# Kernel tuning notes

Hardware: AMD Instinct MI355X
Metric: run time of the kernel (lower is better)

The kernel has to match this reference:

```python
import jax, jax.numpy as jnp
import numpy as np

H = 16
LN_EPS = 1e-5


def setup_inputs() -> dict:
    key = jax.random.key(0)
    ks = jax.random.split(key, 8)
    B, N, D = 2, 2048, 1024
    s = D ** -0.5
    return {
        "q_s": jax.random.normal(ks[0], (B, N, D), jnp.float32),
        "pos_emb": jax.random.normal(ks[1], (B, N, D), jnp.float32),
        "Wq": jax.random.normal(ks[2], (D, D), jnp.float32) * s,
        "Wk": jax.random.normal(ks[3], (D, D), jnp.float32) * s,
        "Wv": jax.random.normal(ks[4], (D, D), jnp.float32) * s,
        "Wo": jax.random.normal(ks[5], (D, D), jnp.float32) * s,
        "bo": jnp.zeros((D,), jnp.float32),
        "ln_g": jnp.ones((D,), jnp.float32),
        "ln_b": jnp.zeros((D,), jnp.float32),
    }


def _split_heads(t):
    b, n, d = t.shape
    return t.reshape(b, n, H, d // H).transpose(0, 2, 1, 3)  # b h n d


def reference(q_s, pos_emb, Wq, Wk, Wv, Wo, bo, ln_g, ln_b):
    # self-attention: k_s = v_s = q_s
    q = _split_heads(q_s @ Wq)
    k = _split_heads(q_s @ Wk)
    v = _split_heads(q_s @ Wv)
    p = _split_heads(pos_emb)
    scale = q.shape[-1] ** -0.5
    # content-content + content-position attention logits: [b,h,i,j]
    att = (jnp.einsum('bhid,bhjd->bhij', q, k) + jnp.einsum('bhid,bhjd->bhij', q, p)) * scale
    att = jax.nn.softmax(att, axis=-1)
    o = jnp.einsum('bhij,bhjd->bhid', att, v)
    b, h, n, d = o.shape
    o = o.transpose(0, 2, 1, 3).reshape(b, n, h * d)
    o = o @ Wo + bo  # out_layer (dropout rate 0 -> identity)
    x = o + q_s  # residual
    mu = jnp.mean(x, axis=-1, keepdims=True)
    var = jnp.var(x, axis=-1, keepdims=True)
    return (x - mu) * jax.lax.rsqrt(var + LN_EPS) * ln_g + ln_b
```

## Files before the change

kernel.cpp:

```cpp
#include <hip/hip_runtime.h>
#include <hip/hip_bf16.h>
#include <stdint.h>

typedef unsigned short u16;
typedef unsigned int u32;
typedef short s16x8 __attribute__((ext_vector_type(8)));
typedef short s16x4 __attribute__((ext_vector_type(4)));
typedef float f32x4 __attribute__((ext_vector_type(4)));

#define MFMA(a, b, c) __builtin_amdgcn_mfma_f32_16x16x32_bf16((a), (b), (c), 0, 0, 0)

__device__ __forceinline__ float bf2f(u16 h) {
  u32 u = ((u32)h) << 16;
  float f;
  __builtin_memcpy(&f, &u, 4);
  return f;
}

__device__ __forceinline__ u16 f2bf_rte(float f) {
  __hip_bfloat16 h = __float2bfloat16(f);
  u16 u;
  __builtin_memcpy(&u, &h, 2);
  return u;
}

__device__ __forceinline__ void gload16(const u16* g, u16* l) {
  __builtin_amdgcn_global_load_lds((const __attribute__((address_space(1))) u32*)g,
                                   (__attribute__((address_space(3))) u32*)l, 16, 0, 0);
}

__global__ __launch_bounds__(256) void k_cvt(const float* __restrict__ in,
                                             u16* __restrict__ out, int n8) {
  int i = blockIdx.x * 256 + threadIdx.x;
  if (i >= n8) return;
  const f32x4* p = (const f32x4*)(in + (size_t)i * 8);
  f32x4 a = p[0], b = p[1];
  s16x8 o;
  for (int k = 0; k < 4; ++k) o[k] = (short)f2bf_rte(a[k]);
  for (int k = 0; k < 4; ++k) o[4 + k] = (short)f2bf_rte(b[k]);
  *(s16x8*)(out + (size_t)i * 8) = o;
}

__global__ __launch_bounds__(256) void k_prep_pos(const float* __restrict__ pos,
                                                  u16* __restrict__ Pp) {
  const int t = threadIdx.x;
  const int bh = blockIdx.y, b = bh >> 4, h = bh & 15;
  const int n = blockIdx.x * 64 + (t >> 2);
  const int d0 = (t & 3) * 16;
  const float* src = &pos[((size_t)(b * 2048 + n)) * 1024 + h * 64 + d0];
  u16* dst = &Pp[((size_t)bh * 2048 + n) * 64 + d0];
  f32x4 a = *(const f32x4*)src;
  f32x4 bq = *(const f32x4*)(src + 4);
  f32x4 c = *(const f32x4*)(src + 8);
  f32x4 dq = *(const f32x4*)(src + 12);
  s16x8 o0, o1;
  for (int i = 0; i < 4; ++i) {
    o0[i] = (short)f2bf_rte(a[i]);
    o0[4 + i] = (short)f2bf_rte(bq[i]);
    o1[i] = (short)f2bf_rte(c[i]);
    o1[4 + i] = (short)f2bf_rte(dq[i]);
  }
  *(s16x8*)dst = o0;
  *(s16x8*)(dst + 8) = o1;
}

__global__ __launch_bounds__(256) void k_transpose_w(const float* __restrict__ W0,
                                                     const float* __restrict__ W1,
                                                     const float* __restrict__ W2,
                                                     const float* __restrict__ W3,
                                                     u16* __restrict__ out) {
  const int z = blockIdx.z;
  const float* in = (z == 0) ? W0 : (z == 1) ? W1 : (z == 2) ? W2 : W3;
  u16* o = out + (size_t)z * 1024 * 1024;
  __shared__ u16 tile[64][65];
  const int t = threadIdx.x, tx = t & 63, ty = t >> 6;
  const int r0 = blockIdx.y * 64, c0 = blockIdx.x * 64;
  for (int rr = 0; rr < 16; ++rr) {
    int row = rr * 4 + ty;
    tile[row][tx] = f2bf_rte(in[(size_t)(r0 + row) * 1024 + c0 + tx]);
  }
  __syncthreads();
  for (int rr = 0; rr < 16; ++rr) {
    int row = rr * 4 + ty;
    o[(size_t)(c0 + row) * 1024 + r0 + tx] = tile[tx][row];
  }
}

__global__ __launch_bounds__(256) void k_transpose_v(const u16* __restrict__ V,
                                                     u16* __restrict__ Vt) {
  __shared__ u16 tile[64][65];
  const int t = threadIdx.x, tx = t & 63, ty = t >> 6;
  const int j0 = blockIdx.x * 64;
  const int bh = blockIdx.y;
  const u16* src = V + (size_t)bh * 2048 * 64;
  u16* dst = Vt + (size_t)bh * 64 * 2048;
  for (int rr = 0; rr < 16; ++rr) {
    int row = rr * 4 + ty;
    tile[row][tx] = src[(size_t)(j0 + row) * 64 + tx];
  }
  __syncthreads();
  for (int rr = 0; rr < 16; ++rr) {
    int d = rr * 4 + ty;
    dst[(size_t)d * 2048 + j0 + tx] = tile[tx][d];
  }
}

__global__ __launch_bounds__(256) void k_qkv_gemm(const u16* __restrict__ X,
                                                  const u16* __restrict__ WT,
                                                  const u16* __restrict__ Pp,
                                                  u16* __restrict__ Qh,
                                                  u16* __restrict__ Kh,
                                                  u16* __restrict__ Vh) {
  __shared__ u16 As[3][4096];
  __shared__ u16 Bs[3][4096];
  const int t = threadIdx.x;
  const int lane = t & 63, wid = t >> 6;
  const int wr = wid >> 1, wc = wid & 1;
  const int g = lane >> 4, lr = lane & 15;
  const int lin = blockIdx.y * 24 + blockIdx.x;
  const int swz = (lin & 7) * 96 + (lin >> 3);
  const int m0 = (swz / 24) * 128, n0 = (swz % 24) * 128;

  const int srcRow = t >> 2;
  const int srcKsw = ((t & 3) * 8) ^ (((t >> 3) & 3) << 3);
  const u16* aSrc = &X[(size_t)(m0 + srcRow) * 1024 + srcKsw];
  const u16* bSrc = &WT[(size_t)(n0 + srcRow) * 1024 + srcKsw];

  const int csw = (g * 8) ^ (((lr >> 1) & 3) << 3);

  f32x4 acc[4][4] = {};

#define QKV_STAGE(buf, k0)                                   \
  {                                                          \
    gload16(aSrc + (k0), &As[buf][wid * 512]);               \
    gload16(aSrc + 65536 + (k0), &As[buf][wid * 512 + 2048]);\
    gload16(bSrc + (k0), &Bs[buf][wid * 512]);               \
    gload16(bSrc + 65536 + (k0), &Bs[buf][wid * 512 + 2048]);\
  }

  QKV_STAGE(0, 0);
  QKV_STAGE(1, 32);
  QKV_STAGE(2, 64);
  for (int k = 0; k < 32; ++k) {
    if (k < 30) {
      asm volatile("s_waitcnt vmcnt(8)" ::: "memory");
    } else if (k == 30) {
      asm volatile("s_waitcnt vmcnt(4)" ::: "memory");
    } else {
      asm volatile("s_waitcnt vmcnt(0)" ::: "memory");
    }
    __builtin_amdgcn_sched_barrier(0);
    __builtin_amdgcn_s_barrier();
    const int cur = k % 3;
    s16x8 a[4], b[4];
#pragma unroll
    for (int mi = 0; mi < 4; ++mi)
      a[mi] = *(const s16x8*)&As[cur][(wr * 64 + mi * 16 + lr) * 32 + csw];
#pragma unroll
    for (int nj = 0; nj < 4; ++nj)
      b[nj] = *(const s16x8*)&Bs[cur][(wc * 64 + nj * 16 + lr) * 32 + csw];
#pragma unroll
    for (int mi = 0; mi < 4; ++mi)
#pragma unroll
      for (int nj = 0; nj < 4; ++nj)
        acc[mi][nj] = MFMA(a[mi], b[nj], acc[mi][nj]);
    __builtin_amdgcn_s_barrier();
    if (k < 29) QKV_STAGE(cur, (k + 3) * 32);
  }
#undef QKV_STAGE

  const float QSCALE = 0.125f * 1.44269504f;
  for (int mi = 0; mi < 4; ++mi) {
    for (int nj = 0; nj < 4; ++nj) {
      const int n_g = n0 + wc * 64 + nj * 16 + lr;
      const int buf = n_g >> 10;
      const int col = n_g & 1023;
      const int h = col >> 6, d = col & 63;
      u16* dst = (buf == 0) ? Qh : ((buf == 1) ? Kh : Vh);
      for (int r = 0; r < 4; ++r) {
        const int row = m0 + wr * 64 + mi * 16 + g * 4 + r;
        const int b = row >> 11, n = row & 2047;
        const size_t off = (size_t)((b * 16 + h) * 2048 + n) * 64 + d;
        float v = acc[mi][nj][r];
        if (buf == 1) v += bf2f(Pp[off]);
        if (buf == 0) v *= QSCALE;
        dst[off] = f2bf_rte(v);
      }
    }
  }
}

__global__ __launch_bounds__(512, 4) void k_attn(const u16* __restrict__ Qh,
                                                 const u16* __restrict__ Kh,
                                                 const u16* __restrict__ Vt,
                                                 u16* __restrict__ Oh) {
  const int t = threadIdx.x, lane = t & 63, wid = t >> 6;
  const int g = lane >> 4, lr = lane & 15;
  const int hid = blockIdx.x;
  const int lid = (hid & 7) * 64 + (hid >> 3);
  const int bh = lid >> 4, itile = lid & 15;
  const int i0 = itile * 128 + wid * 16;

  __shared__ char Ks[4][8192];
  __shared__ char Vs[4][8192];

  const u16* Qp = Qh + (size_t)bh * 2048 * 64;
  const u16* Kp = Kh + (size_t)bh * 2048 * 64;
  const u16* Vp = Vt + (size_t)bh * 64 * 2048;

  s16x8 aq[2];
  aq[0] = *(const s16x8*)&Qp[(size_t)(i0 + lr) * 64 + g * 8];
  aq[1] = *(const s16x8*)&Qp[(size_t)(i0 + lr) * 64 + 32 + g * 8];

  f32x4 oa[4] = {};
  float ms = -1e30f, ls = 0.f;

  const int srow = t >> 3;
  const int sch = (t & 7) * 16;
  const int schS = sch ^ ((srow & 7) << 4);
  const u16* kB = &Kp[(size_t)srow * 64 + (schS >> 1)];
  const u16* vB = &Vp[(size_t)srow * 2048 + (schS >> 1)];

#define ATTN_STAGE(p)                                          \
  {                                                            \
    gload16(kB + (size_t)(p) * 4096, (u16*)Ks[(p) & 3] + wid * 512); \
    gload16(vB + (size_t)(p) * 64, (u16*)Vs[(p) & 3] + wid * 512);   \
  }

  ATTN_STAGE(0);
  ATTN_STAGE(1);
  ATTN_STAGE(2);

  for (int tt = 0; tt < 32; ++tt) {
    if (tt < 30) {
      asm volatile("s_waitcnt vmcnt(4)" ::: "memory");
    } else if (tt == 30) {
      asm volatile("s_waitcnt vmcnt(2)" ::: "memory");
    } else {
      asm volatile("s_waitcnt vmcnt(0)" ::: "memory");
    }
    __builtin_amdgcn_sched_barrier(0);
    __builtin_amdgcn_s_barrier();
    if (tt < 29) ATTN_STAGE(tt + 3);

    const char* Kc = Ks[tt & 3];
    const char* Vc = Vs[tt & 3];

    f32x4 s[4] = {};
    __builtin_amdgcn_s_setprio(1);
#pragma unroll
    for (int jf = 0; jf < 4; ++jf) {
      const int row = jf * 16 + lr;
      const int bw = (row & 7) << 4;
      s16x8 bk0 = *(const s16x8*)(Kc + ((row * 128 + g * 16) ^ bw));
      s16x8 bk1 = *(const s16x8*)(Kc + ((row * 128 + 64 + g * 16) ^ bw));
      s[jf] = MFMA(bk0, aq[0], s[jf]);
      s[jf] = MFMA(bk1, aq[1], s[jf]);
    }
    __builtin_amdgcn_s_setprio(0);

    float tl = s[0][0];
#pragma unroll
    for (int jf = 0; jf < 4; ++jf)
#pragma unroll
      for (int r = 0; r < 4; ++r)
        if (jf | r) tl = fmaxf(tl, s[jf][r]);
    if (!__all(tl <= ms + 8.f)) {
      float tm = fmaxf(tl, __shfl_xor(tl, 16, 64));
      tm = fmaxf(tm, __shfl_xor(tm, 32, 64));
      float mn = fmaxf(ms, tm);
      float al = __builtin_amdgcn_exp2f(ms - mn);
      ls *= al;
      ms = mn;
#pragma unroll
      for (int r = 0; r < 4; ++r) {
        float ab = __shfl(al, g * 4 + r, 64);
#pragma unroll
        for (int df = 0; df < 4; ++df) oa[df][r] *= ab;
      }
    }

#pragma unroll
    for (int jf = 0; jf < 4; ++jf)
#pragma unroll
      for (int r = 0; r < 4; ++r) {
        float p = __builtin_amdgcn_exp2f(s[jf][r] - ms);
        s[jf][r] = p;
        ls += p;
      }

    u32 pk[4][2];
#pragma unroll
    for (int jf = 0; jf < 4; ++jf) {
      asm("v_cvt_pk_bf16_f32 %0, %1, %2" : "=v"(pk[jf][0]) : "v"(s[jf][0]), "v"(s[jf][1]));
      asm("v_cvt_pk_bf16_f32 %0, %1, %2" : "=v"(pk[jf][1]) : "v"(s[jf][2]), "v"(s[jf][3]));
    }

    s16x8 pa[2];
#pragma unroll
    for (int c = 0; c < 2; ++c) {
      u32 w_[4];
#pragma unroll
      for (int wl = 0; wl < 2; ++wl) {
        u32 A = pk[2 * c][wl], B = pk[2 * c + 1][wl];
        asm("v_permlane32_swap_b32 %0, %1" : "+v"(A), "+v"(B));
        asm("v_permlane16_swap_b32 %0, %1" : "+v"(A), "+v"(B));
        w_[wl] = A;
        w_[2 + wl] = B;
      }
      __builtin_memcpy(&pa[c], w_, 16);
    }

    __builtin_amdgcn_s_setprio(1);
#pragma unroll
    for (int df = 0; df < 4; ++df) {
      const int row = df * 16 + lr;
      const int bw = (row & 7) << 4;
      s16x8 bv0 = *(const s16x8*)(Vc + ((row * 128 + g * 16) ^ bw));
      s16x8 bv1 = *(const s16x8*)(Vc + ((row * 128 + 64 + g * 16) ^ bw));
      oa[df] = MFMA(pa[0], bv0, oa[df]);
      oa[df] = MFMA(pa[1], bv1, oa[df]);
    }
    __builtin_amdgcn_s_setprio(0);
  }
#undef ATTN_STAGE

  ls += __shfl_xor(ls, 16, 64);
  ls += __shfl_xor(ls, 32, 64);
  float lb[4];
#pragma unroll
  for (int r = 0; r < 4; ++r) lb[r] = __shfl(ls, g * 4 + r, 64);

  u16* Op = Oh + (size_t)bh * 2048 * 64;
#pragma unroll
  for (int df = 0; df < 4; ++df)
#pragma unroll
    for (int r = 0; r < 4; ++r) {
      const int row0 = i0 + g * 4 + r;
      Op[(size_t)row0 * 64 + df * 16 + lr] = f2bf_rte(oa[df][r] / lb[r]);
    }
}

__global__ __launch_bounds__(256) void k_out_gemm(const u16* __restrict__ Oh,
                                                  const u16* __restrict__ WTo,
                                                  const float* __restrict__ bo,
                                                  const u16* __restrict__ qsb,
                                                  float* __restrict__ X) {
  __shared__ u16 As[3][4096];
  __shared__ u16 Bs[3][4096];
  const int t = threadIdx.x;
  const int lane = t & 63, wid = t >> 6;
  const int wr = wid >> 1, wc = wid & 1;
  const int g = lane >> 4, lr = lane & 15;
  const int lin = blockIdx.y * 8 + blockIdx.x;
  const int swz = (lin & 7) * 32 + (lin >> 3);
  const int m0 = (swz / 8) * 128, n0 = (swz % 8) * 128;

  const int srcRow = t >> 2;
  const int srcKsw = ((t & 3) * 8) ^ (((t >> 3) & 3) << 3);
  const int rg = m0 + srcRow, bb0 = rg >> 11, nn0 = rg & 2047;
  const int rg2 = rg + 64, bb2 = rg2 >> 11, nn2 = rg2 & 2047;
  const u16* bSrc = &WTo[(size_t)(n0 + srcRow) * 1024 + srcKsw];
  const int csw = (g * 8) ^ (((lr >> 1) & 3) << 3);

  f32x4 acc[4][4] = {};

#define OUT_STAGE(buf, k0)                                                        \
  {                                                                               \
    const int h_ = (k0) >> 6, d_ = ((k0) & 63) + srcKsw;                          \
    gload16(&Oh[((size_t)(bb0 * 16 + h_) * 2048 + nn0) * 64 + d_],                \
            &As[buf][wid * 512]);                                                 \
    gload16(&Oh[((size_t)(bb2 * 16 + h_) * 2048 + nn2) * 64 + d_],                \
            &As[buf][wid * 512 + 2048]);                                          \
    gload16(bSrc + (k0), &Bs[buf][wid * 512]);                                    \
    gload16(bSrc + 65536 + (k0), &Bs[buf][wid * 512 + 2048]);                     \
  }

  OUT_STAGE(0, 0);
  OUT_STAGE(1, 32);
  OUT_STAGE(2, 64);
  for (int k = 0; k < 32; ++k) {
    if (k < 30) {
      asm volatile("s_waitcnt vmcnt(8)" ::: "memory");
    } else if (k == 30) {
      asm volatile("s_waitcnt vmcnt(4)" ::: "memory");
    } else {
      asm volatile("s_waitcnt vmcnt(0)" ::: "memory");
    }
    __builtin_amdgcn_sched_barrier(0);
    __builtin_amdgcn_s_barrier();
    const int cur = k % 3;
    s16x8 a[4], b[4];
#pragma unroll
    for (int mi = 0; mi < 4; ++mi)
      a[mi] = *(const s16x8*)&As[cur][(wr * 64 + mi * 16 + lr) * 32 + csw];
#pragma unroll
    for (int nj = 0; nj < 4; ++nj)
      b[nj] = *(const s16x8*)&Bs[cur][(wc * 64 + nj * 16 + lr) * 32 + csw];
#pragma unroll
    for (int mi = 0; mi < 4; ++mi)
#pragma unroll
      for (int nj = 0; nj < 4; ++nj)
        acc[mi][nj] = MFMA(a[mi], b[nj], acc[mi][nj]);
    __builtin_amdgcn_s_barrier();
    if (k < 29) OUT_STAGE(cur, (k + 3) * 32);
  }
#undef OUT_STAGE

  for (int mi = 0; mi < 4; ++mi) {
    for (int nj = 0; nj < 4; ++nj) {
      const int col = n0 + wc * 64 + nj * 16 + lr;
      for (int r = 0; r < 4; ++r) {
        const int row = m0 + wr * 64 + mi * 16 + g * 4 + r;
        float v = acc[mi][nj][r] + bo[col] + bf2f(qsb[(size_t)row * 1024 + col]);
        X[(size_t)row * 1024 + col] = v;
      }
    }
  }
}

__global__ __launch_bounds__(256) void k_ln(const float* __restrict__ X,
                                            const float* __restrict__ gg,
                                            const float* __restrict__ bb,
                                            float* __restrict__ out) {
  const int row = blockIdx.x, t = threadIdx.x;
  const int wid = t >> 6, lane = t & 63;
  const float* xr = X + (size_t)row * 1024;
  f32x4 x = *(const f32x4*)&xr[t * 4];
  float s1 = x[0] + x[1] + x[2] + x[3];
  float s2 = x[0] * x[0] + x[1] * x[1] + x[2] * x[2] + x[3] * x[3];
  for (int off = 32; off > 0; off >>= 1) {
    s1 += __shfl_down(s1, off, 64);
    s2 += __shfl_down(s2, off, 64);
  }
  __shared__ float red[2][4];
  if (lane == 0) { red[0][wid] = s1; red[1][wid] = s2; }
  __syncthreads();
  s1 = red[0][0] + red[0][1] + red[0][2] + red[0][3];
  s2 = red[1][0] + red[1][1] + red[1][2] + red[1][3];
  const float mu = s1 * (1.f / 1024.f);
  const float var = s2 * (1.f / 1024.f) - mu * mu;
  const float rstd = rsqrtf(var + 1e-5f);
  f32x4 gv = *(const f32x4*)&gg[t * 4];
  f32x4 bv = *(const f32x4*)&bb[t * 4];
  f32x4 ov;
  for (int i = 0; i < 4; ++i) ov[i] = (x[i] - mu) * rstd * gv[i] + bv[i];
  *(f32x4*)&out[(size_t)row * 1024 + t * 4] = ov;
}

extern "C" void kernel_launch(void* const* d_in, const int* in_sizes, int n_in,
                              void* d_out, int out_size, void* d_ws, size_t ws_size,
                              hipStream_t stream) {
  (void)in_sizes; (void)n_in; (void)out_size; (void)ws_size;
  const float* q_s = (const float*)d_in[0];
  const float* pos = (const float*)d_in[1];
  const float* Wq = (const float*)d_in[2];
  const float* Wk = (const float*)d_in[3];
  const float* Wv = (const float*)d_in[4];
  const float* Wo = (const float*)d_in[5];
  const float* bo = (const float*)d_in[6];
  const float* lng = (const float*)d_in[7];
  const float* lnb = (const float*)d_in[8];
  float* out = (float*)d_out;

  u16* ws = (u16*)d_ws;
  const size_t MB1 = 1024 * 1024;
  u16* WT  = ws;
  u16* Xbf = ws + 4 * MB1;
  u16* Qh  = Xbf + 4 * MB1;
  u16* Kh  = Qh + 4 * MB1;
  u16* Vh  = Kh + 4 * MB1;
  u16* Vt  = Vh + 4 * MB1;
  u16* Oh  = Vt + 4 * MB1;
  u16* Pp  = Oh;
  float* Xb = (float*)Qh;

  dim3 blk(256);
  k_cvt<<<dim3(2048), blk, 0, stream>>>(q_s, Xbf, 4 * MB1 / 8);
  k_prep_pos<<<dim3(32, 32), blk, 0, stream>>>(pos, Pp);
  k_transpose_w<<<dim3(16, 16, 4), blk, 0, stream>>>(Wq, Wk, Wv, Wo, WT);
  k_qkv_gemm<<<dim3(24, 32), blk, 0, stream>>>(Xbf, WT, Pp, Qh, Kh, Vh);
  k_transpose_v<<<dim3(32, 32), blk, 0, stream>>>(Vh, Vt);
  k_attn<<<dim3(512), dim3(512), 0, stream>>>(Qh, Kh, Vt, Oh);
  k_out_gemm<<<dim3(8, 32), blk, 0, stream>>>(Oh, WT + 3 * MB1, bo, Xbf, Xb);
  k_ln<<<4096, blk, 0, stream>>>(Xb, lng, lnb, out);
}
```

Measured before the change: 147.5 us.

## Unroll attention KV loop by four with constant buffer indices and tree reductions

The 32-iteration KV tile loop of the attention kernel is restructured into 7 blocks of 4 unrolled iterations plus a peeled epilogue of four. Each iteration then uses a compile-time LDS buffer index, and the per-iteration branching on wait counts and stage issue goes away. Row-max and row-sum reductions become balanced trees instead of serial chains, and the s_setprio hints around the MFMA groups are dropped. The larger unrolled body gives the scheduler more room but raises code size and possibly register pressure.

```diff
diff --git a/kernel.cpp b/kernel.cpp
--- a/kernel.cpp
+++ b/kernel.cpp
@@ -221,108 +221,120 @@
   const u16* kB = &Kp[(size_t)srow * 64 + (schS >> 1)];
   const u16* vB = &Vp[(size_t)srow * 2048 + (schS >> 1)];
 
-#define ATTN_STAGE(p)                                          \
-  {                                                            \
+#define ATTN_STAGE(p)                                                \
+  {                                                                  \
     gload16(kB + (size_t)(p) * 4096, (u16*)Ks[(p) & 3] + wid * 512); \
     gload16(vB + (size_t)(p) * 64, (u16*)Vs[(p) & 3] + wid * 512);   \
+  }
+
+#define ATTN_BODY(BUF)                                                         \
+  {                                                                            \
+    const char* Kc = Ks[BUF];                                                  \
+    const char* Vc = Vs[BUF];                                                  \
+    f32x4 s[4] = {};                                                           \
+    _Pragma("unroll") for (int jf = 0; jf < 4; ++jf) {                         \
+      const int row = jf * 16 + lr;                                            \
+      const int bw = (row & 7) << 4;                                           \
+      s16x8 bk0 = *(const s16x8*)(Kc + ((row * 128 + g * 16) ^ bw));           \
+      s16x8 bk1 = *(const s16x8*)(Kc + ((row * 128 + 64 + g * 16) ^ bw));      \
+      s[jf] = MFMA(bk0, aq[0], s[jf]);                                         \
+      s[jf] = MFMA(bk1, aq[1], s[jf]);                                         \
+    }                                                                          \
+                                                       \
+    float mj[4];                                                               \
+    _Pragma("unroll") for (int jf = 0; jf < 4; ++jf)                           \
+        mj[jf] = fmaxf(fmaxf(s[jf][0], s[jf][1]), fmaxf(s[jf][2], s[jf][3]));  \
+    float tl = fmaxf(fmaxf(mj[0], mj[1]), fmaxf(mj[2], mj[3]));                \
+    if (!__all(tl <= ms + 8.f)) {                                              \
+      float tm = fmaxf(tl, __shfl_xor(tl, 16, 64));                            \
+      tm = fmaxf(tm, __shfl_xor(tm, 32, 64));                                  \
+      float mn = fmaxf(ms, tm);                                                \
+      float al = __builtin_amdgcn_exp2f(ms - mn);                              \
+      ls *= al;                                                                \
+      ms = mn;                                                                 \
+      _Pragma("unroll") for (int r = 0; r < 4; ++r) {                          \
+        float ab = __shfl(al, g * 4 + r, 64);                                  \
+        _Pragma("unroll") for (int df = 0; df < 4; ++df) oa[df][r] *= ab;      \
+      }                                                                        \
+    }                                                                          \
+                                            \
+    float pj[4];                                                               \
+    _Pragma("unroll") for (int jf = 0; jf < 4; ++jf) {                         \
+      _Pragma("unroll") for (int r = 0; r < 4; ++r)                            \
+          s[jf][r] = __builtin_amdgcn_exp2f(s[jf][r] - ms);                    \
+      pj[jf] = (s[jf][0] + s[jf][1]) + (s[jf][2] + s[jf][3]);                  \
+    }                                                                          \
+    ls += (pj[0] + pj[1]) + (pj[2] + pj[3]);                                   \
+    u32 pk[4][2];                                                              \
+    _Pragma("unroll") for (int jf = 0; jf < 4; ++jf) {                         \
+      asm("v_cvt_pk_bf16_f32 %0, %1, %2"                                       \
+          : "=v"(pk[jf][0]) : "v"(s[jf][0]), "v"(s[jf][1]));                   \
+      asm("v_cvt_pk_bf16_f32 %0, %1, %2"                                       \
+          : "=v"(pk[jf][1]) : "v"(s[jf][2]), "v"(s[jf][3]));                   \
+    }                                                                          \
+    s16x8 pa[2];                                                               \
+    _Pragma("unroll") for (int c = 0; c < 2; ++c) {                            \
+      u32 w_[4];                                                               \
+      _Pragma("unroll") for (int wl = 0; wl < 2; ++wl) {                       \
+        u32 A = pk[2 * c][wl], B = pk[2 * c + 1][wl];                          \
+        asm("v_permlane32_swap_b32 %0, %1" : "+v"(A), "+v"(B));                \
+        asm("v_permlane16_swap_b32 %0, %1" : "+v"(A), "+v"(B));                \
+        w_[wl] = A;                                                            \
+        w_[2 + wl] = B;                                                        \
+      }                                                                        \
+      __builtin_memcpy(&pa[c], w_, 16);                                        \
+    }                                                                          \
+    _Pragma("unroll") for (int df = 0; df < 4; ++df) {                         \
+      const int row = df * 16 + lr;                                            \
+      const int bw = (row & 7) << 4;                                           \
+      s16x8 bv0 = *(const s16x8*)(Vc + ((row * 128 + g * 16) ^ bw));           \
+      s16x8 bv1 = *(const s16x8*)(Vc + ((row * 128 + 64 + g * 16) ^ bw));      \
+      oa[df] = MFMA(pa[0], bv0, oa[df]);                                       \
+      oa[df] = MFMA(pa[1], bv1, oa[df]);                                       \
+    }                                                                          \
   }
 
   ATTN_STAGE(0);
   ATTN_STAGE(1);
   ATTN_STAGE(2);
 
-  for (int tt = 0; tt < 32; ++tt) {
-    if (tt < 30) {
+  for (int tb = 0; tb < 7; ++tb) {
+#pragma unroll
+    for (int ti = 0; ti < 4; ++ti) {
+      const int tt = tb * 4 + ti;
       asm volatile("s_waitcnt vmcnt(4)" ::: "memory");
-    } else if (tt == 30) {
-      asm volatile("s_waitcnt vmcnt(2)" ::: "memory");
-    } else {
-      asm volatile("s_waitcnt vmcnt(0)" ::: "memory");
-    }
-    __builtin_amdgcn_sched_barrier(0);
-    __builtin_amdgcn_s_barrier();
-    if (tt < 29) ATTN_STAGE(tt + 3);
-
-    const char* Kc = Ks[tt & 3];
-    const char* Vc = Vs[tt & 3];
-
-    f32x4 s[4] = {};
-    __builtin_amdgcn_s_setprio(1);
-#pragma unroll
-    for (int jf = 0; jf < 4; ++jf) {
-      const int row = jf * 16 + lr;
-      const int bw = (row & 7) << 4;
-      s16x8 bk0 = *(const s16x8*)(Kc + ((row * 128 + g * 16) ^ bw));
-      s16x8 bk1 = *(const s16x8*)(Kc + ((row * 128 + 64 + g * 16) ^ bw));
-      s[jf] = MFMA(bk0, aq[0], s[jf]);
-      s[jf] = MFMA(bk1, aq[1], s[jf]);
-    }
-    __builtin_amdgcn_s_setprio(0);
-
-    float tl = s[0][0];
-#pragma unroll
-    for (int jf = 0; jf < 4; ++jf)
-#pragma unroll
-      for (int r = 0; r < 4; ++r)
-        if (jf | r) tl = fmaxf(tl, s[jf][r]);
-    if (!__all(tl <= ms + 8.f)) {
-      float tm = fmaxf(tl, __shfl_xor(tl, 16, 64));
-      tm = fmaxf(tm, __shfl_xor(tm, 32, 64));
-      float mn = fmaxf(ms, tm);
-      float al = __builtin_amdgcn_exp2f(ms - mn);
-      ls *= al;
-      ms = mn;
-#pragma unroll
-      for (int r = 0; r < 4; ++r) {
-        float ab = __shfl(al, g * 4 + r, 64);
-#pragma unroll
-        for (int df = 0; df < 4; ++df) oa[df][r] *= ab;
-      }
-    }
-
-#pragma unroll
-    for (int jf = 0; jf < 4; ++jf)
-#pragma unroll
-      for (int r = 0; r < 4; ++r) {
-        float p = __builtin_amdgcn_exp2f(s[jf][r] - ms);
-        s[jf][r] = p;
-        ls += p;
-      }
-
-    u32 pk[4][2];
-#pragma unroll
-    for (int jf = 0; jf < 4; ++jf) {
-      asm("v_cvt_pk_bf16_f32 %0, %1, %2" : "=v"(pk[jf][0]) : "v"(s[jf][0]), "v"(s[jf][1]));
-      asm("v_cvt_pk_bf16_f32 %0, %1, %2" : "=v"(pk[jf][1]) : "v"(s[jf][2]), "v"(s[jf][3]));
-    }
-
-    s16x8 pa[2];
-#pragma unroll
-    for (int c = 0; c < 2; ++c) {
-      u32 w_[4];
-#pragma unroll
-      for (int wl = 0; wl < 2; ++wl) {
-        u32 A = pk[2 * c][wl], B = pk[2 * c + 1][wl];
-        asm("v_permlane32_swap_b32 %0, %1" : "+v"(A), "+v"(B));
-        asm("v_permlane16_swap_b32 %0, %1" : "+v"(A), "+v"(B));
-        w_[wl] = A;
-        w_[2 + wl] = B;
-      }
-      __builtin_memcpy(&pa[c], w_, 16);
-    }
-
-    __builtin_amdgcn_s_setprio(1);
-#pragma unroll
-    for (int df = 0; df < 4; ++df) {
-      const int row = df * 16 + lr;
-      const int bw = (row & 7) << 4;
-      s16x8 bv0 = *(const s16x8*)(Vc + ((row * 128 + g * 16) ^ bw));
-      s16x8 bv1 = *(const s16x8*)(Vc + ((row * 128 + 64 + g * 16) ^ bw));
-      oa[df] = MFMA(pa[0], bv0, oa[df]);
-      oa[df] = MFMA(pa[1], bv1, oa[df]);
-    }
-    __builtin_amdgcn_s_setprio(0);
-  }
+      __builtin_amdgcn_sched_barrier(0);
+      __builtin_amdgcn_s_barrier();
+      ATTN_STAGE(tt + 3);
+      ATTN_BODY(ti);
+    }
+  }
+  {
+    asm volatile("s_waitcnt vmcnt(4)" ::: "memory");
+    __builtin_amdgcn_sched_barrier(0);
+    __builtin_amdgcn_s_barrier();
+    ATTN_STAGE(31);
+    ATTN_BODY(0);
+  }
+  {
+    asm volatile("s_waitcnt vmcnt(4)" ::: "memory");
+    __builtin_amdgcn_sched_barrier(0);
+    __builtin_amdgcn_s_barrier();
+    ATTN_BODY(1);
+  }
+  {
+    asm volatile("s_waitcnt vmcnt(2)" ::: "memory");
+    __builtin_amdgcn_sched_barrier(0);
+    __builtin_amdgcn_s_barrier();
+    ATTN_BODY(2);
+  }
+  {
+    asm volatile("s_waitcnt vmcnt(0)" ::: "memory");
+    __builtin_amdgcn_sched_barrier(0);
+    __builtin_amdgcn_s_barrier();
+    ATTN_BODY(3);
+  }
+#undef ATTN_BODY
 #undef ATTN_STAGE
 
   ls += __shfl_xor(ls, 16, 64);
```

Measured after the change: 147.5 us. No clear change (-0.0%).
